# Kernel optimization log

Measured on AMD Instinct MI355X. Metric: run time of the kernel, lower is better.

Reference implementation:

```python
import jax, jax.numpy as jnp
import numpy as np


def setup_inputs() -> dict:
    key = jax.random.key(0)
    ks = jax.random.split(key, 10)
    B, N, F, H = 4, 512, 64, 4
    x = jax.random.normal(ks[0], (B, N, F), dtype=jnp.float32)
    adj = jax.random.uniform(ks[1], (N, N), dtype=jnp.float32)
    s = 1.0 / np.sqrt(F)
    Wq = jax.random.normal(ks[2], (F, F * H), dtype=jnp.float32) * s
    bq = jnp.zeros((F * H,), dtype=jnp.float32)
    Wk = jax.random.normal(ks[3], (F, F * H), dtype=jnp.float32) * s
    bk = jnp.zeros((F * H,), dtype=jnp.float32)
    Wlin = jax.random.normal(ks[4], (H, F), dtype=jnp.float32) * (1.0 / np.sqrt(H))
    blin = jnp.zeros((F,), dtype=jnp.float32)
    Wfc = jax.random.normal(ks[5], (F, F), dtype=jnp.float32) * s
    bfc = jnp.zeros((F,), dtype=jnp.float32)
    return {"x": x, "adj": adj, "Wq": Wq, "bq": bq, "Wk": Wk, "bk": bk,
            "Wlin": Wlin, "blin": blin, "Wfc": Wfc, "bfc": bfc}


def reference(x, adj, Wq, bq, Wk, bk, Wlin, blin, Wfc, bfc):
    B, N, F = x.shape
    H = Wlin.shape[0]
    # multi-head attention matrix (value projection is computed but unused in the original)
    q = (x @ Wq + bq).reshape(B, N, H, F)  # [B,N,H,F]
    k = (x @ Wk + bk).reshape(B, N, H, F)
    scores = jnp.einsum('bihf,bjhf->bhij', q, k) / jnp.sqrt(jnp.float32(F))
    attn = jax.nn.softmax(scores, axis=-1)  # [B,H,N,N]
    # linear over heads: [B,N,N,H] @ [H,F] -> [B,N,N,F]
    SV2 = jnp.einsum('bhij,hf->bijf', attn, Wlin) + blin
    # symmetric normalization of (adj + I)
    A = adj + jnp.eye(N, dtype=adj.dtype)
    d = jnp.sum(A, axis=1) ** -0.5
    noradj = d[:, None] * A * d[None, :]  # [N,N]
    # sum over dim 1 (source index i) of noradj[i,j]*SV2[b,i,j,f]*x[b,j,f]
    S = jnp.einsum('ij,bijf->bjf', noradj, SV2)
    sx = x * S  # [B,N,F]
    out = jnp.einsum('ij,bjf->bif', noradj, sx)
    out = out @ Wfc + bfc
    return jax.nn.relu(out)
```

## Files before the change

kernel.cpp:

```cpp
#include <hip/hip_runtime.h>
#include <math.h>

#define NN 512
#define FF 64
#define HH 4


__global__ __launch_bounds__(64) void k_dinv(const float* __restrict__ adj,
                                             float* __restrict__ dinv,
                                             float* __restrict__ T) {
    int i = blockIdx.x;
    int lane = threadIdx.x;
    float acc = 0.f;
#pragma unroll
    for (int k = 0; k < 8; ++k) acc += adj[i * NN + k * 64 + lane];
    for (int o = 32; o > 0; o >>= 1) acc += __shfl_xor(acc, o);
    if (lane == 0) dinv[i] = 1.0f / sqrtf(acc + 1.0f);
    if (i < 128) T[i * 64 + lane] = 0.f;
}

__global__ __launch_bounds__(256) void k_csum_part(const float* __restrict__ adj,
                                                   const float* __restrict__ dinv,
                                                   float* __restrict__ psum) {
    int ic = blockIdx.x;
    int j0 = threadIdx.x, j1 = threadIdx.x + 256;
    float a0 = 0.f, a1 = 0.f;
#pragma unroll
    for (int ii = 0; ii < 16; ++ii) {
        int i = ic * 16 + ii;
        float di = dinv[i];
        a0 = fmaf(di, adj[i * NN + j0], a0);
        a1 = fmaf(di, adj[i * NN + j1], a1);
    }
    psum[ic * NN + j0] = a0;
    psum[ic * NN + j1] = a1;
}

__global__ __launch_bounds__(256) void k_qk(const float* __restrict__ x,
                                            const float* __restrict__ Wq,
                                            const float* __restrict__ bq,
                                            const float* __restrict__ Wk,
                                            const float* __restrict__ bk,
                                            float* __restrict__ q_t,
                                            float* __restrict__ kT) {
    __shared__ float x_lds[4][64];
    int blk = blockIdx.x;
    int b = blk >> 8, rest = blk & 255, isK = rest >> 7, itile = rest & 127;
    int i0 = itile * 4;
    int tid = threadIdx.x;
    x_lds[tid >> 6][tid & 63] = x[((long)b * NN + i0 + (tid >> 6)) * FF + (tid & 63)];
    __syncthreads();
    const float* W = isK ? Wk : Wq;
    const float* bias = isK ? bk : bq;
    int col = tid, h = col >> 6, f = col & 63;
    float bv = bias[col];
    float a0 = bv, a1 = bv, a2 = bv, a3 = bv;
    for (int cc = 0; cc < 64; ++cc) {
        float w = W[cc * 256 + col];
        a0 = fmaf(x_lds[0][cc], w, a0);
        a1 = fmaf(x_lds[1][cc], w, a1);
        a2 = fmaf(x_lds[2][cc], w, a2);
        a3 = fmaf(x_lds[3][cc], w, a3);
    }
    int bh = b * HH + h;
    if (!isK) {
        long base = ((long)bh * NN + i0) * FF + f;
        q_t[base] = a0; q_t[base + FF] = a1; q_t[base + 2 * FF] = a2; q_t[base + 3 * FF] = a3;
    } else {
        long base = ((long)bh * FF + f) * NN + i0;
        *(float4*)(kT + base) = make_float4(a0, a1, a2, a3);
    }
}

__global__ __launch_bounds__(256) void k_scores(const float* __restrict__ q_t,
                                                const float* __restrict__ kT,
                                                const float* __restrict__ adj,
                                                const float* __restrict__ dinv,
                                                float* __restrict__ T) {
    __shared__ float q_lds[8][64];
    __shared__ float red[8][4];
    __shared__ float red2[8][4];
    int blk = blockIdx.x;
    int itile = blk & 63, h = (blk >> 6) & 3, b = blk >> 8;
    int bh = b * HH + h;
    int i0 = itile * 8;
    int tid = threadIdx.x;
#pragma unroll
    for (int k = 0; k < 2; ++k) {
        int idx = k * 256 + tid;
        q_lds[idx >> 6][idx & 63] = q_t[((long)bh * NN + i0 + (idx >> 6)) * FF + (idx & 63)];
    }
    __syncthreads();
    int j0 = tid, j1 = tid + 256;
    const float* kb = kT + (long)bh * FF * NN;
    float s0[8], s1[8];
#pragma unroll
    for (int r = 0; r < 8; ++r) { s0[r] = 0.f; s1[r] = 0.f; }
    for (int f4 = 0; f4 < 64; f4 += 4) {
        float kv0[4], kv1[4];
#pragma unroll
        for (int u = 0; u < 4; ++u) {
            kv0[u] = kb[(f4 + u) * NN + j0];
            kv1[u] = kb[(f4 + u) * NN + j1];
        }
#pragma unroll
        for (int r = 0; r < 8; ++r) {
            float4 qv = *(const float4*)&q_lds[r][f4];
            s0[r] = fmaf(qv.x, kv0[0], s0[r]);
            s0[r] = fmaf(qv.y, kv0[1], s0[r]);
            s0[r] = fmaf(qv.z, kv0[2], s0[r]);
            s0[r] = fmaf(qv.w, kv0[3], s0[r]);
            s1[r] = fmaf(qv.x, kv1[0], s1[r]);
            s1[r] = fmaf(qv.y, kv1[1], s1[r]);
            s1[r] = fmaf(qv.z, kv1[2], s1[r]);
            s1[r] = fmaf(qv.w, kv1[3], s1[r]);
        }
    }
    const float scale = 0.125f;
    int wave = tid >> 6, lane = tid & 63;
    float m[8];
#pragma unroll
    for (int r = 0; r < 8; ++r) {
        float v = fmaxf(s0[r], s1[r]);
        for (int o = 32; o > 0; o >>= 1) v = fmaxf(v, __shfl_xor(v, o));
        if (lane == 0) red[r][wave] = v;
    }
    __syncthreads();
#pragma unroll
    for (int r = 0; r < 8; ++r)
        m[r] = fmaxf(fmaxf(red[r][0], red[r][1]), fmaxf(red[r][2], red[r][3]));
#pragma unroll
    for (int r = 0; r < 8; ++r) {
        s0[r] = expf((s0[r] - m[r]) * scale);
        s1[r] = expf((s1[r] - m[r]) * scale);
        float v = s0[r] + s1[r];
        for (int o = 32; o > 0; o >>= 1) v += __shfl_xor(v, o);
        if (lane == 0) red2[r][wave] = v;
    }
    __syncthreads();
    float dj0 = dinv[j0], dj1 = dinv[j1];
    float pw0 = 0.f, pw1 = 0.f;
#pragma unroll
    for (int r = 0; r < 8; ++r) {
        float Zi = 1.0f / (red2[r][0] + red2[r][1] + red2[r][2] + red2[r][3]);
        int gi = i0 + r;
        float di = dinv[gi];
        float a0 = adj[(long)gi * NN + j0] + (gi == j0 ? 1.f : 0.f);
        float a1 = adj[(long)gi * NN + j1] + (gi == j1 ? 1.f : 0.f);
        pw0 += di * a0 * s0[r] * Zi;
        pw1 += di * a1 * s1[r] * Zi;
    }
    atomicAdd(&T[bh * NN + j0], pw0 * dj0);
    atomicAdd(&T[bh * NN + j1], pw1 * dj1);
}

__global__ __launch_bounds__(256) void k_sxd(const float* __restrict__ x,
                                             const float* __restrict__ T,
                                             const float* __restrict__ Wlin,
                                             const float* __restrict__ blin,
                                             const float* __restrict__ psum,
                                             const float* __restrict__ dinv,
                                             float* __restrict__ sxd) {
    int t = blockIdx.x * 256 + threadIdx.x;
    int f = t & 63;
    int j = (t >> 6) & (NN - 1);
    int b = t >> 15;
    float cs = 0.f;
#pragma unroll
    for (int p = 0; p < 32; ++p) cs += psum[p * NN + j];
    float dj = dinv[j];
    float cj = dj * (cs + dj);
    float S = blin[f] * cj;
#pragma unroll
    for (int h = 0; h < HH; ++h) S += T[(b * HH + h) * NN + j] * Wlin[h * FF + f];
    sxd[t] = x[t] * S * dj;
}

__global__ __launch_bounds__(512) void k_final(const float* __restrict__ sxd,
                                               const float* __restrict__ adj,
                                               const float* __restrict__ dinv,
                                               const float* __restrict__ Wfc,
                                               const float* __restrict__ bfc,
                                               float* __restrict__ out) {
    __shared__ float part[2][4][64];
    __shared__ float m_lds[4][64];
    __shared__ float part2[2][4][64];
    int blk = blockIdx.x;
    int b = blk >> 7, itile = blk & 127;
    int i0 = itile * 4;
    int tid = threadIdx.x;
    int f = tid & 63, r = (tid >> 6) & 3, jc = tid >> 8;
    int i = i0 + r;
    const float* sb = sxd + (long)b * NN * FF + f;
    const float* ar = adj + (long)i * NN;
    float acc = 0.f;
    int jbeg = jc * 256;
#pragma unroll 8
    for (int j = jbeg; j < jbeg + 256; ++j) {
        acc = fmaf(ar[j], sb[(long)j * FF], acc);
    }
    if ((i >> 8) == jc) acc += sb[(long)i * FF];
    part[jc][r][f] = acc;
    __syncthreads();
    if (jc == 0) m_lds[r][f] = (part[0][r][f] + part[1][r][f]) * dinv[i];
    __syncthreads();
    float o = 0.f;
    int c0 = jc * 32;
#pragma unroll
    for (int cc = 0; cc < 32; ++cc) {
        o = fmaf(m_lds[r][c0 + cc], Wfc[(c0 + cc) * FF + f], o);
    }
    part2[jc][r][f] = o;
    __syncthreads();
    if (jc == 0) {
        float oo = part2[0][r][f] + part2[1][r][f] + bfc[f];
        out[((long)b * NN + i) * FF + f] = fmaxf(oo, 0.f);
    }
}

extern "C" void kernel_launch(void* const* d_in, const int* in_sizes, int n_in,
                              void* d_out, int out_size, void* d_ws, size_t ws_size,
                              hipStream_t stream) {
    const float* x    = (const float*)d_in[0];
    const float* adj  = (const float*)d_in[1];
    const float* Wq   = (const float*)d_in[2];
    const float* bq   = (const float*)d_in[3];
    const float* Wk   = (const float*)d_in[4];
    const float* bk   = (const float*)d_in[5];
    const float* Wlin = (const float*)d_in[6];
    const float* blin = (const float*)d_in[7];
    const float* Wfc  = (const float*)d_in[8];
    const float* bfc  = (const float*)d_in[9];
    float* out = (float*)d_out;

    float* ws   = (float*)d_ws;
    float* dinv = ws;
    float* psum = ws + 512;
    float* T    = ws + 16896;
    float* q_t  = ws + 25088;
    float* kT   = ws + 2122240;
    float* sxd  = ws + 4219392;

    k_dinv<<<dim3(512), dim3(64), 0, stream>>>(adj, dinv, T);
    k_csum_part<<<dim3(32), dim3(256), 0, stream>>>(adj, dinv, psum);
    k_qk<<<dim3(1024), dim3(256), 0, stream>>>(x, Wq, bq, Wk, bk, q_t, kT);
    k_scores<<<dim3(1024), dim3(256), 0, stream>>>(q_t, kT, adj, dinv, T);
    k_sxd<<<dim3(512), dim3(256), 0, stream>>>(x, T, Wlin, blin, psum, dinv, sxd);
    k_final<<<dim3(512), dim3(512), 0, stream>>>(sxd, adj, dinv, Wfc, bfc, out);
}
```

Measured before the change: 120.7 us.

## Fuse all stages into one persistent cooperative kernel with grid syncs

Replaces the six separate kernel launches with a single cooperative persistent kernel. The grid is sized from occupancy and capped at 1024 blocks, and stages are separated by grid.sync(). The final aggregation stage is retiled to two rows per 256-thread block with four j-chunks instead of four rows per 512-thread block. This removes launch gaps and per-kernel tail effects, at the cost of grid-wide barriers and a host-side occupancy query on every launch.

```diff
diff --git a/kernel.cpp b/kernel.cpp
--- a/kernel.cpp
+++ b/kernel.cpp
@@ -1,220 +1,222 @@
 #include <hip/hip_runtime.h>
+#include <hip/hip_cooperative_groups.h>
 #include <math.h>
+
+namespace cg = cooperative_groups;
 
 #define NN 512
 #define FF 64
 #define HH 4
 
 
-__global__ __launch_bounds__(64) void k_dinv(const float* __restrict__ adj,
-                                             float* __restrict__ dinv,
-                                             float* __restrict__ T) {
-    int i = blockIdx.x;
-    int lane = threadIdx.x;
-    float acc = 0.f;
-#pragma unroll
-    for (int k = 0; k < 8; ++k) acc += adj[i * NN + k * 64 + lane];
-    for (int o = 32; o > 0; o >>= 1) acc += __shfl_xor(acc, o);
-    if (lane == 0) dinv[i] = 1.0f / sqrtf(acc + 1.0f);
-    if (i < 128) T[i * 64 + lane] = 0.f;
-}
-
-__global__ __launch_bounds__(256) void k_csum_part(const float* __restrict__ adj,
-                                                   const float* __restrict__ dinv,
-                                                   float* __restrict__ psum) {
-    int ic = blockIdx.x;
-    int j0 = threadIdx.x, j1 = threadIdx.x + 256;
-    float a0 = 0.f, a1 = 0.f;
-#pragma unroll
-    for (int ii = 0; ii < 16; ++ii) {
-        int i = ic * 16 + ii;
-        float di = dinv[i];
-        a0 = fmaf(di, adj[i * NN + j0], a0);
-        a1 = fmaf(di, adj[i * NN + j1], a1);
-    }
-    psum[ic * NN + j0] = a0;
-    psum[ic * NN + j1] = a1;
-}
-
-__global__ __launch_bounds__(256) void k_qk(const float* __restrict__ x,
-                                            const float* __restrict__ Wq,
-                                            const float* __restrict__ bq,
-                                            const float* __restrict__ Wk,
-                                            const float* __restrict__ bk,
-                                            float* __restrict__ q_t,
-                                            float* __restrict__ kT) {
+__global__ __launch_bounds__(256, 4) void k_fused(
+    const float* __restrict__ x, const float* __restrict__ adj,
+    const float* __restrict__ Wq, const float* __restrict__ bq,
+    const float* __restrict__ Wk, const float* __restrict__ bk,
+    const float* __restrict__ Wlin, const float* __restrict__ blin,
+    const float* __restrict__ Wfc, const float* __restrict__ bfc,
+    float* __restrict__ out,
+    float* __restrict__ dinv, float* __restrict__ psum,
+    float* __restrict__ T, float* __restrict__ q_t,
+    float* __restrict__ kT, float* __restrict__ sxd)
+{
+    cg::grid_group grid = cg::this_grid();
+    const int blk = blockIdx.x, tid = threadIdx.x;
+    const int nb = gridDim.x;
+    const int wv = tid >> 6, lane = tid & 63;
+
     __shared__ float x_lds[4][64];
-    int blk = blockIdx.x;
-    int b = blk >> 8, rest = blk & 255, isK = rest >> 7, itile = rest & 127;
-    int i0 = itile * 4;
-    int tid = threadIdx.x;
-    x_lds[tid >> 6][tid & 63] = x[((long)b * NN + i0 + (tid >> 6)) * FF + (tid & 63)];
-    __syncthreads();
-    const float* W = isK ? Wk : Wq;
-    const float* bias = isK ? bk : bq;
-    int col = tid, h = col >> 6, f = col & 63;
-    float bv = bias[col];
-    float a0 = bv, a1 = bv, a2 = bv, a3 = bv;
-    for (int cc = 0; cc < 64; ++cc) {
-        float w = W[cc * 256 + col];
-        a0 = fmaf(x_lds[0][cc], w, a0);
-        a1 = fmaf(x_lds[1][cc], w, a1);
-        a2 = fmaf(x_lds[2][cc], w, a2);
-        a3 = fmaf(x_lds[3][cc], w, a3);
-    }
-    int bh = b * HH + h;
-    if (!isK) {
-        long base = ((long)bh * NN + i0) * FF + f;
-        q_t[base] = a0; q_t[base + FF] = a1; q_t[base + 2 * FF] = a2; q_t[base + 3 * FF] = a3;
-    } else {
-        long base = ((long)bh * FF + f) * NN + i0;
-        *(float4*)(kT + base) = make_float4(a0, a1, a2, a3);
-    }
-}
-
-__global__ __launch_bounds__(256) void k_scores(const float* __restrict__ q_t,
-                                                const float* __restrict__ kT,
-                                                const float* __restrict__ adj,
-                                                const float* __restrict__ dinv,
-                                                float* __restrict__ T) {
     __shared__ float q_lds[8][64];
     __shared__ float red[8][4];
     __shared__ float red2[8][4];
-    int blk = blockIdx.x;
-    int itile = blk & 63, h = (blk >> 6) & 3, b = blk >> 8;
-    int bh = b * HH + h;
-    int i0 = itile * 8;
-    int tid = threadIdx.x;
-#pragma unroll
-    for (int k = 0; k < 2; ++k) {
-        int idx = k * 256 + tid;
-        q_lds[idx >> 6][idx & 63] = q_t[((long)bh * NN + i0 + (idx >> 6)) * FF + (idx & 63)];
-    }
-    __syncthreads();
-    int j0 = tid, j1 = tid + 256;
-    const float* kb = kT + (long)bh * FF * NN;
-    float s0[8], s1[8];
-#pragma unroll
-    for (int r = 0; r < 8; ++r) { s0[r] = 0.f; s1[r] = 0.f; }
-    for (int f4 = 0; f4 < 64; f4 += 4) {
-        float kv0[4], kv1[4];
-#pragma unroll
-        for (int u = 0; u < 4; ++u) {
-            kv0[u] = kb[(f4 + u) * NN + j0];
-            kv1[u] = kb[(f4 + u) * NN + j1];
-        }
+    __shared__ float part[4][2][64];
+    __shared__ float m_lds[2][64];
+    __shared__ float part2[4][2][64];
+
+    for (int gw = blk * 4 + wv; gw < NN; gw += nb * 4) {
+        float acc = 0.f;
+#pragma unroll
+        for (int k = 0; k < 8; ++k) acc += adj[gw * NN + k * 64 + lane];
+        for (int o = 32; o > 0; o >>= 1) acc += __shfl_xor(acc, o);
+        if (lane == 0) dinv[gw] = 1.0f / sqrtf(acc + 1.0f);
+    }
+    for (int t = blk * 256 + tid; t < 4 * HH * NN; t += nb * 256) T[t] = 0.f;
+
+    for (int u = blk; u < 1024; u += nb) {
+        int b = u >> 8, rest = u & 255, isK = rest >> 7, itile = rest & 127;
+        int i0 = itile * 4;
+        __syncthreads();
+        x_lds[tid >> 6][tid & 63] = x[((long)b * NN + i0 + (tid >> 6)) * FF + (tid & 63)];
+        __syncthreads();
+        const float* W = isK ? Wk : Wq;
+        float bv = (isK ? bk : bq)[tid];
+        float a0 = bv, a1 = bv, a2 = bv, a3 = bv;
+        for (int cc = 0; cc < 64; ++cc) {
+            float w = W[cc * 256 + tid];
+            a0 = fmaf(x_lds[0][cc], w, a0);
+            a1 = fmaf(x_lds[1][cc], w, a1);
+            a2 = fmaf(x_lds[2][cc], w, a2);
+            a3 = fmaf(x_lds[3][cc], w, a3);
+        }
+        int h = tid >> 6, f = tid & 63;
+        int bh = b * HH + h;
+        if (!isK) {
+            long base = ((long)bh * NN + i0) * FF + f;
+            q_t[base] = a0; q_t[base + FF] = a1;
+            q_t[base + 2 * FF] = a2; q_t[base + 3 * FF] = a3;
+        } else {
+            long base = ((long)bh * FF + f) * NN + i0;
+            *(float4*)(kT + base) = make_float4(a0, a1, a2, a3);
+        }
+    }
+    grid.sync();
+
+    for (int u = blk; u < 32; u += nb) {
+        int j0 = tid, j1 = tid + 256;
+        float a0 = 0.f, a1 = 0.f;
+#pragma unroll
+        for (int ii = 0; ii < 16; ++ii) {
+            int i = u * 16 + ii;
+            float di = dinv[i];
+            a0 = fmaf(di, adj[i * NN + j0], a0);
+            a1 = fmaf(di, adj[i * NN + j1], a1);
+        }
+        psum[u * NN + j0] = a0;
+        psum[u * NN + j1] = a1;
+    }
+
+    for (int u = blk; u < 1024; u += nb) {
+        int itile = u & 63, h = (u >> 6) & 3, b = u >> 8;
+        int bh = b * HH + h, i0 = itile * 8;
+        __syncthreads();
+#pragma unroll
+        for (int k = 0; k < 2; ++k) {
+            int idx = k * 256 + tid;
+            q_lds[idx >> 6][idx & 63] =
+                q_t[((long)bh * NN + i0 + (idx >> 6)) * FF + (idx & 63)];
+        }
+        __syncthreads();
+        int j0 = tid, j1 = tid + 256;
+        const float* kb = kT + (long)bh * FF * NN;
+        float s0[8], s1[8];
+#pragma unroll
+        for (int r = 0; r < 8; ++r) { s0[r] = 0.f; s1[r] = 0.f; }
+        for (int f4 = 0; f4 < 64; f4 += 4) {
+            float kv0[4], kv1[4];
+#pragma unroll
+            for (int uu = 0; uu < 4; ++uu) {
+                kv0[uu] = kb[(f4 + uu) * NN + j0];
+                kv1[uu] = kb[(f4 + uu) * NN + j1];
+            }
+#pragma unroll
+            for (int r = 0; r < 8; ++r) {
+                float4 qv = *(const float4*)&q_lds[r][f4];
+                s0[r] = fmaf(qv.x, kv0[0], s0[r]);
+                s0[r] = fmaf(qv.y, kv0[1], s0[r]);
+                s0[r] = fmaf(qv.z, kv0[2], s0[r]);
+                s0[r] = fmaf(qv.w, kv0[3], s0[r]);
+                s1[r] = fmaf(qv.x, kv1[0], s1[r]);
+                s1[r] = fmaf(qv.y, kv1[1], s1[r]);
+                s1[r] = fmaf(qv.z, kv1[2], s1[r]);
+                s1[r] = fmaf(qv.w, kv1[3], s1[r]);
+            }
+        }
+        const float scale = 0.125f;
+        float m[8];
 #pragma unroll
         for (int r = 0; r < 8; ++r) {
-            float4 qv = *(const float4*)&q_lds[r][f4];
-            s0[r] = fmaf(qv.x, kv0[0], s0[r]);
-            s0[r] = fmaf(qv.y, kv0[1], s0[r]);
-            s0[r] = fmaf(qv.z, kv0[2], s0[r]);
-            s0[r] = fmaf(qv.w, kv0[3], s0[r]);
-            s1[r] = fmaf(qv.x, kv1[0], s1[r]);
-            s1[r] = fmaf(qv.y, kv1[1], s1[r]);
-            s1[r] = fmaf(qv.z, kv1[2], s1[r]);
-            s1[r] = fmaf(qv.w, kv1[3], s1[r]);
-        }
-    }
-    const float scale = 0.125f;
-    int wave = tid >> 6, lane = tid & 63;
-    float m[8];
-#pragma unroll
-    for (int r = 0; r < 8; ++r) {
-        float v = fmaxf(s0[r], s1[r]);
-        for (int o = 32; o > 0; o >>= 1) v = fmaxf(v, __shfl_xor(v, o));
-        if (lane == 0) red[r][wave] = v;
-    }
-    __syncthreads();
-#pragma unroll
-    for (int r = 0; r < 8; ++r)
-        m[r] = fmaxf(fmaxf(red[r][0], red[r][1]), fmaxf(red[r][2], red[r][3]));
-#pragma unroll
-    for (int r = 0; r < 8; ++r) {
-        s0[r] = expf((s0[r] - m[r]) * scale);
-        s1[r] = expf((s1[r] - m[r]) * scale);
-        float v = s0[r] + s1[r];
-        for (int o = 32; o > 0; o >>= 1) v += __shfl_xor(v, o);
-        if (lane == 0) red2[r][wave] = v;
-    }
-    __syncthreads();
-    float dj0 = dinv[j0], dj1 = dinv[j1];
-    float pw0 = 0.f, pw1 = 0.f;
-#pragma unroll
-    for (int r = 0; r < 8; ++r) {
-        float Zi = 1.0f / (red2[r][0] + red2[r][1] + red2[r][2] + red2[r][3]);
-        int gi = i0 + r;
-        float di = dinv[gi];
-        float a0 = adj[(long)gi * NN + j0] + (gi == j0 ? 1.f : 0.f);
-        float a1 = adj[(long)gi * NN + j1] + (gi == j1 ? 1.f : 0.f);
-        pw0 += di * a0 * s0[r] * Zi;
-        pw1 += di * a1 * s1[r] * Zi;
-    }
-    atomicAdd(&T[bh * NN + j0], pw0 * dj0);
-    atomicAdd(&T[bh * NN + j1], pw1 * dj1);
-}
-
-__global__ __launch_bounds__(256) void k_sxd(const float* __restrict__ x,
-                                             const float* __restrict__ T,
-                                             const float* __restrict__ Wlin,
-                                             const float* __restrict__ blin,
-                                             const float* __restrict__ psum,
-                                             const float* __restrict__ dinv,
-                                             float* __restrict__ sxd) {
-    int t = blockIdx.x * 256 + threadIdx.x;
-    int f = t & 63;
-    int j = (t >> 6) & (NN - 1);
-    int b = t >> 15;
-    float cs = 0.f;
-#pragma unroll
-    for (int p = 0; p < 32; ++p) cs += psum[p * NN + j];
-    float dj = dinv[j];
-    float cj = dj * (cs + dj);
-    float S = blin[f] * cj;
-#pragma unroll
-    for (int h = 0; h < HH; ++h) S += T[(b * HH + h) * NN + j] * Wlin[h * FF + f];
-    sxd[t] = x[t] * S * dj;
-}
-
-__global__ __launch_bounds__(512) void k_final(const float* __restrict__ sxd,
-                                               const float* __restrict__ adj,
-                                               const float* __restrict__ dinv,
-                                               const float* __restrict__ Wfc,
-                                               const float* __restrict__ bfc,
-                                               float* __restrict__ out) {
-    __shared__ float part[2][4][64];
-    __shared__ float m_lds[4][64];
-    __shared__ float part2[2][4][64];
-    int blk = blockIdx.x;
-    int b = blk >> 7, itile = blk & 127;
-    int i0 = itile * 4;
-    int tid = threadIdx.x;
-    int f = tid & 63, r = (tid >> 6) & 3, jc = tid >> 8;
-    int i = i0 + r;
-    const float* sb = sxd + (long)b * NN * FF + f;
-    const float* ar = adj + (long)i * NN;
-    float acc = 0.f;
-    int jbeg = jc * 256;
-#pragma unroll 8
-    for (int j = jbeg; j < jbeg + 256; ++j) {
-        acc = fmaf(ar[j], sb[(long)j * FF], acc);
-    }
-    if ((i >> 8) == jc) acc += sb[(long)i * FF];
-    part[jc][r][f] = acc;
-    __syncthreads();
-    if (jc == 0) m_lds[r][f] = (part[0][r][f] + part[1][r][f]) * dinv[i];
-    __syncthreads();
-    float o = 0.f;
-    int c0 = jc * 32;
-#pragma unroll
-    for (int cc = 0; cc < 32; ++cc) {
-        o = fmaf(m_lds[r][c0 + cc], Wfc[(c0 + cc) * FF + f], o);
-    }
-    part2[jc][r][f] = o;
-    __syncthreads();
-    if (jc == 0) {
-        float oo = part2[0][r][f] + part2[1][r][f] + bfc[f];
-        out[((long)b * NN + i) * FF + f] = fmaxf(oo, 0.f);
+            float v = fmaxf(s0[r], s1[r]);
+            for (int o = 32; o > 0; o >>= 1) v = fmaxf(v, __shfl_xor(v, o));
+            if (lane == 0) red[r][wv] = v;
+        }
+        __syncthreads();
+#pragma unroll
+        for (int r = 0; r < 8; ++r)
+            m[r] = fmaxf(fmaxf(red[r][0], red[r][1]), fmaxf(red[r][2], red[r][3]));
+#pragma unroll
+        for (int r = 0; r < 8; ++r) {
+            s0[r] = expf((s0[r] - m[r]) * scale);
+            s1[r] = expf((s1[r] - m[r]) * scale);
+            float v = s0[r] + s1[r];
+            for (int o = 32; o > 0; o >>= 1) v += __shfl_xor(v, o);
+            if (lane == 0) red2[r][wv] = v;
+        }
+        __syncthreads();
+        float dj0 = dinv[j0], dj1 = dinv[j1];
+        float pw0 = 0.f, pw1 = 0.f;
+#pragma unroll
+        for (int r = 0; r < 8; ++r) {
+            float Zi = 1.0f / (red2[r][0] + red2[r][1] + red2[r][2] + red2[r][3]);
+            int gi = i0 + r;
+            float di = dinv[gi];
+            float a0 = adj[(long)gi * NN + j0] + (gi == j0 ? 1.f : 0.f);
+            float a1 = adj[(long)gi * NN + j1] + (gi == j1 ? 1.f : 0.f);
+            pw0 += di * a0 * s0[r] * Zi;
+            pw1 += di * a1 * s1[r] * Zi;
+        }
+        atomicAdd(&T[bh * NN + j0], pw0 * dj0);
+        atomicAdd(&T[bh * NN + j1], pw1 * dj1);
+    }
+    grid.sync();
+
+    for (int t = blk * 256 + tid; t < 4 * NN * FF; t += nb * 256) {
+        int f = t & 63, j = (t >> 6) & (NN - 1), b = t >> 15;
+        float cs = 0.f;
+#pragma unroll
+        for (int p = 0; p < 32; ++p) cs += psum[p * NN + j];
+        float dj = dinv[j];
+        float cj = dj * (cs + dj);
+        float S = blin[f] * cj;
+#pragma unroll
+        for (int h = 0; h < HH; ++h) S += T[(b * HH + h) * NN + j] * Wlin[h * FF + f];
+        sxd[t] = x[t] * S * dj;
+    }
+    grid.sync();
+
+    for (int u = blk; u < 1024; u += nb) {
+        int b = u >> 8, itile = u & 255;
+        int i0 = itile * 2;
+        int f = tid & 63, jc = tid >> 6;
+        const float* sb = sxd + (long)b * NN * FF + f;
+        const float* ar0 = adj + (long)i0 * NN;
+        const float* ar1 = ar0 + NN;
+        float a0 = 0.f, a1 = 0.f;
+        int jb = jc * 128;
+#pragma unroll 4
+        for (int j = jb; j < jb + 128; ++j) {
+            float v = sb[(long)j * FF];
+            a0 = fmaf(ar0[j], v, a0);
+            a1 = fmaf(ar1[j], v, a1);
+        }
+        if ((i0 >> 7) == jc) a0 += sb[(long)i0 * FF];
+        if (((i0 + 1) >> 7) == jc) a1 += sb[(long)(i0 + 1) * FF];
+        __syncthreads();
+        part[jc][0][f] = a0;
+        part[jc][1][f] = a1;
+        __syncthreads();
+        if (jc == 0) {
+            m_lds[0][f] = (part[0][0][f] + part[1][0][f] + part[2][0][f] + part[3][0][f]) * dinv[i0];
+            m_lds[1][f] = (part[0][1][f] + part[1][1][f] + part[2][1][f] + part[3][1][f]) * dinv[i0 + 1];
+        }
+        __syncthreads();
+        float o0 = 0.f, o1 = 0.f;
+        int c0 = jc * 16;
+#pragma unroll
+        for (int cc = 0; cc < 16; ++cc) {
+            float w = Wfc[(c0 + cc) * FF + f];
+            o0 = fmaf(m_lds[0][c0 + cc], w, o0);
+            o1 = fmaf(m_lds[1][c0 + cc], w, o1);
+        }
+        part2[jc][0][f] = o0;
+        part2[jc][1][f] = o1;
+        __syncthreads();
+        if (jc == 0) {
+            float bb = bfc[f];
+            float r0 = part2[0][0][f] + part2[1][0][f] + part2[2][0][f] + part2[3][0][f] + bb;
+            float r1 = part2[0][1][f] + part2[1][1][f] + part2[2][1][f] + part2[3][1][f] + bb;
+            out[((long)b * NN + i0) * FF + f]     = fmaxf(r0, 0.f);
+            out[((long)b * NN + i0 + 1) * FF + f] = fmaxf(r1, 0.f);
+        }
     }
 }
 
@@ -241,10 +243,16 @@
     float* kT   = ws + 2122240;
     float* sxd  = ws + 4219392;
 
-    k_dinv<<<dim3(512), dim3(64), 0, stream>>>(adj, dinv, T);
-    k_csum_part<<<dim3(32), dim3(256), 0, stream>>>(adj, dinv, psum);
-    k_qk<<<dim3(1024), dim3(256), 0, stream>>>(x, Wq, bq, Wk, bk, q_t, kT);
-    k_scores<<<dim3(1024), dim3(256), 0, stream>>>(q_t, kT, adj, dinv, T);
-    k_sxd<<<dim3(512), dim3(256), 0, stream>>>(x, T, Wlin, blin, psum, dinv, sxd);
-    k_final<<<dim3(512), dim3(512), 0, stream>>>(sxd, adj, dinv, Wfc, bfc, out);
+    int nbpcu = 0;
+    hipOccupancyMaxActiveBlocksPerMultiprocessor(&nbpcu, k_fused, 256, 0);
+    if (nbpcu < 1) nbpcu = 1;
+    long grid = (long)nbpcu * 256;
+    if (grid > 1024) grid = 1024;
+
+    void* args[] = {(void*)&x, (void*)&adj, (void*)&Wq, (void*)&bq, (void*)&Wk,
+                    (void*)&bk, (void*)&Wlin, (void*)&blin, (void*)&Wfc, (void*)&bfc,
+                    (void*)&out, (void*)&dinv, (void*)&psum, (void*)&T,
+                    (void*)&q_t, (void*)&kT, (void*)&sxd};
+    hipLaunchCooperativeKernel((void*)k_fused, dim3((unsigned)grid), dim3(256),
+                               args, 0, stream);
 }
```

After: 318.1 us. 164% more time.
